# Kernel optimization log

Hardware: AMD Instinct MI355X
Metric: run time of the kernel (lower is better)

Reference implementation:

```python
import jax, jax.numpy as jnp
import numpy as np

NUM_HEADS = 16
NEG_BIG = -1.0e9


def setup_inputs() -> dict:
    key = jax.random.key(0)
    k1, k2, k3 = jax.random.split(key, 3)
    B, S, D = 2, 2048, 1024
    x = jax.random.normal(k1, (B, S, D), dtype=jnp.float32)
    qkv_weights = jax.random.normal(k2, (D, 3 * D), dtype=jnp.float32) * (1.0 / np.sqrt(D))
    output_weights = jax.random.normal(k3, (D, D), dtype=jnp.float32) * (1.0 / np.sqrt(D))
    return {"x": x, "qkv_weights": qkv_weights, "output_weights": output_weights}


def reference(x, qkv_weights, output_weights):
    B, S, D = x.shape
    H = NUM_HEADS
    hd = D // H
    qkv = jnp.einsum('bsd,de->bse', x, qkv_weights)  # [B,S,3D]
    q, k, v = jnp.split(qkv, 3, axis=-1)
    # [B,H,S,hd]
    q = q.reshape(B, S, H, hd).transpose(0, 2, 1, 3)
    k = k.reshape(B, S, H, hd).transpose(0, 2, 1, 3)
    v = v.reshape(B, S, H, hd).transpose(0, 2, 1, 3)
    scores = jnp.einsum('bhqd,bhkd->bhqk', q, k)  # unscaled, matches original masked path
    # original bug: when masked, softmax is applied to UNSCALED scores with mask
    tril = jnp.tril(jnp.ones((S, S), dtype=scores.dtype))
    masked = scores * tril + NEG_BIG * (1.0 - tril)
    attn = jax.nn.softmax(masked, axis=-1)
    heads = jnp.einsum('bhqk,bhkd->bhqd', attn, v)  # [B,H,S,hd]
    merged = heads.transpose(0, 2, 1, 3).reshape(B, S, D)
    return jnp.einsum('bsd,de->bse', merged, output_weights)
```

## Files before the change

### kernel.cpp

```cpp
#include <hip/hip_runtime.h>
#include <stdint.h>

using u16 = unsigned short;
typedef __attribute__((ext_vector_type(8))) _Float16 half8;
typedef __attribute__((ext_vector_type(4))) float f32x4;
typedef __attribute__((ext_vector_type(4))) unsigned short u16x4;

#define S_LEN 2048
#define D_MODEL 1024
#define NHEAD 16
#define HDIM 64

__device__ __forceinline__ u16 f2h_bits(float f){
    _Float16 h = (_Float16)f;
    return __builtin_bit_cast(u16, h);
}

typedef __attribute__((address_space(1))) void gvoid;
typedef __attribute__((address_space(3))) void lvoid;
__device__ __forceinline__ void gload_lds16(const u16* g, u16* l){
    __builtin_amdgcn_global_load_lds((gvoid*)(uintptr_t)g, (lvoid*)l, 16, 0, 0);
}

__global__ __launch_bounds__(256) void k_cvt_x(const float* __restrict__ x, u16* __restrict__ xh){
    int i = blockIdx.x*256 + threadIdx.x;
    float4 v = reinterpret_cast<const float4*>(x)[i];
    u16x4 o;
    o.x = f2h_bits(v.x); o.y = f2h_bits(v.y); o.z = f2h_bits(v.z); o.w = f2h_bits(v.w);
    reinterpret_cast<u16x4*>(xh)[i] = o;
}

__global__ __launch_bounds__(256) void k_cvt_wT(const float* __restrict__ W, u16* __restrict__ WT,
                                                int K, int N){
    __shared__ float t[32][33];
    int tx = threadIdx.x & 31, ty = threadIdx.x >> 5;
    int n0 = blockIdx.x*32, k0 = blockIdx.y*32;
    #pragma unroll
    for (int i=0;i<4;++i) t[ty+8*i][tx] = W[(size_t)(k0+ty+8*i)*N + n0+tx];
    __syncthreads();
    #pragma unroll
    for (int i=0;i<4;++i) WT[(size_t)(n0+ty+8*i)*K + k0+tx] = f2h_bits(t[tx][ty+8*i]);
}

template<int EPI>
__global__ __launch_bounds__(256) void k_gemm(const u16* __restrict__ A, const u16* __restrict__ BT,
                                              float* __restrict__ Cf, u16* __restrict__ Qh,
                                              u16* __restrict__ Kh, u16* __restrict__ Vt){
    constexpr int Kd = 1024;
    __shared__ u16 As[128*32];
    __shared__ u16 Bs[128*32];
    int nwg = gridDim.x;
    int cpx = nwg >> 3;
    int wg  = ((int)blockIdx.x & 7)*cpx + ((int)blockIdx.x >> 3);
    int tm = wg & 31, tn = wg >> 5;
    int t = threadIdx.x;
    int w = t >> 6, lane = t & 63;
    int lr = lane & 15, lg = lane >> 4;
    int wm = (w>>1)*64, wn = (w&1)*64;
    int m0 = tm*128 + wm, n0 = tn*128 + wn;

    const u16* aG = A  + (size_t)(tm*128 + (t>>2))*Kd + (t&3)*8;
    const u16* bG = BT + (size_t)(tn*128 + (t>>2))*Kd + (t&3)*8;
    u16* aL = As + (t>>2)*32 + (t&3)*8;
    u16* bL = Bs + (t>>2)*32 + (t&3)*8;

    f32x4 acc[4][4];
    #pragma unroll
    for (int i=0;i<4;++i)
        #pragma unroll
        for (int j=0;j<4;++j) acc[i][j] = (f32x4){0.f,0.f,0.f,0.f};

    for (int kk=0; kk<Kd; kk+=32){
        gload_lds16(aG + kk, aL);
        gload_lds16(aG + kk + (size_t)64*Kd, aL + 64*32);
        gload_lds16(bG + kk, bL);
        gload_lds16(bG + kk + (size_t)64*Kd, bL + 64*32);
        __syncthreads();

        half8 av[4], bv[4];
        #pragma unroll
        for (int mf=0;mf<4;++mf) av[mf] = *reinterpret_cast<const half8*>(&As[(wm+mf*16+lr)*32 + lg*8]);
        #pragma unroll
        for (int nf=0;nf<4;++nf) bv[nf] = *reinterpret_cast<const half8*>(&Bs[(wn+nf*16+lr)*32 + lg*8]);
        __builtin_amdgcn_s_setprio(1);
        #pragma unroll
        for (int mf=0;mf<4;++mf)
            #pragma unroll
            for (int nf=0;nf<4;++nf)
                acc[mf][nf] = __builtin_amdgcn_mfma_f32_16x16x32_f16(av[mf], bv[nf], acc[mf][nf], 0,0,0);
        __builtin_amdgcn_s_setprio(0);
        __syncthreads();
    }

    if (EPI == 0){
        #pragma unroll
        for (int mf=0;mf<4;++mf)
            #pragma unroll
            for (int nf=0;nf<4;++nf)
                #pragma unroll
                for (int j=0;j<4;++j)
                    Cf[(size_t)(m0+mf*16+lg*4+j)*D_MODEL + n0+nf*16+lr] = acc[mf][nf][j];
    } else {
        #pragma unroll
        for (int mf=0;mf<4;++mf){
            int r0 = m0 + mf*16 + lg*4;
            int b  = r0 >> 11, s = r0 & 2047;
            #pragma unroll
            for (int nf=0;nf<4;++nf){
                int col = n0 + nf*16 + lr;
                int which = col >> 10;
                int d  = col & 1023;
                int h  = d >> 6, di = d & 63;
                int bh = b*NHEAD + h;
                if (which == 2){
                    u16x4 pv;
                    pv.x = f2h_bits(acc[mf][nf][0]);
                    pv.y = f2h_bits(acc[mf][nf][1]);
                    pv.z = f2h_bits(acc[mf][nf][2]);
                    pv.w = f2h_bits(acc[mf][nf][3]);
                    *reinterpret_cast<u16x4*>(Vt + ((size_t)bh*HDIM + di)*S_LEN + s) = pv;
                } else {
                    u16* dst = (which==0 ? Qh : Kh) + ((size_t)bh*S_LEN + s)*HDIM + di;
                    #pragma unroll
                    for (int j=0;j<4;++j) dst[(size_t)j*HDIM] = f2h_bits(acc[mf][nf][j]);
                }
            }
        }
    }
}

__global__ __launch_bounds__(256,3) void k_attn(const u16* __restrict__ Q, const u16* __restrict__ K,
                                                const u16* __restrict__ Vt, u16* __restrict__ Mg){
    __shared__ u16 Kl[64*64];
    __shared__ u16 Vl[64*64];
    __shared__ u16 plds[4][32][72];
    int t = threadIdx.x;
    int w = t >> 6, lane = t & 63;
    int lr = lane & 15, lg = lane >> 4;
    int blk = blockIdx.x;
    int bh  = blk & 31;
    int g   = blk >> 5;
    int qb  = (g < 8) ? g : 23 - g;
    int q0w = qb*128 + w*32;
    int b = bh >> 4, h = bh & 15;
    const u16* Qp = Q  + (size_t)bh*S_LEN*HDIM;
    const u16* Kp = K  + (size_t)bh*S_LEN*HDIM;
    const u16* Vp = Vt + (size_t)bh*HDIM*S_LEN;

    int c0 = t, c1 = t + 256;
    int r0 = c0 >> 3, s0 = 8*((c0 & 7) ^ (r0 & 7));
    int r1 = c1 >> 3, s1 = 8*((c1 & 7) ^ (r1 & 7));
    const u16* Ks0 = Kp + (size_t)r0*HDIM + s0;
    const u16* Ks1 = Kp + (size_t)r1*HDIM + s1;
    const u16* Vs0 = Vp + (size_t)r0*S_LEN + s0;
    const u16* Vs1 = Vp + (size_t)r1*S_LEN + s1;
    u16* Kd0 = Kl + c0*8; u16* Kd1 = Kl + c1*8;
    u16* Vd0 = Vl + c0*8; u16* Vd1 = Vl + c1*8;

    half8 qf[2][2];
    #pragma unroll
    for (int qi=0;qi<2;++qi)
        #pragma unroll
        for (int ks=0;ks<2;++ks){
            half8 v = *reinterpret_cast<const half8*>(Qp + (size_t)(q0w+qi*16+lr)*HDIM + ks*32 + lg*8);
            #pragma unroll
            for (int j=0;j<8;++j) v[j] = v[j] * (_Float16)1.44269504f;
            qf[qi][ks] = v;
        }

    f32x4 oacc[2][4];
    float mrow[2], lrow[2];
    #pragma unroll
    for (int mf=0;mf<2;++mf){
        #pragma unroll
        for (int nf=0;nf<4;++nf) oacc[mf][nf] = (f32x4){0.f,0.f,0.f,0.f};
        mrow[mf] = -1e30f; lrow[mf] = 0.f;
    }

    int ktb    = 2*qb + 2;
    int lastkt = (q0w + 31) >> 6;

    int swz = (lr & 7)*8;

    for (int kt=0; kt<ktb; ++kt){
        int kbase = kt*64;
        gload_lds16(Ks0 + (size_t)kbase*HDIM, Kd0);
        gload_lds16(Ks1 + (size_t)kbase*HDIM, Kd1);
        gload_lds16(Vs0 + kbase, Vd0);
        gload_lds16(Vs1 + kbase, Vd1);
        __syncthreads();

        if (kt <= lastkt){
            half8 kfr[4][2];
            #pragma unroll
            for (int kf=0;kf<4;++kf)
                #pragma unroll
                for (int ks=0;ks<2;++ks)
                    kfr[kf][ks] = *reinterpret_cast<const half8*>(Kl + (kf*16+lr)*64 + ((ks*32 + lg*8) ^ swz));
            f32x4 sc[4][2];
            #pragma unroll
            for (int kf=0;kf<4;++kf)
                #pragma unroll
                for (int qi=0;qi<2;++qi) sc[kf][qi] = (f32x4){0.f,0.f,0.f,0.f};
            __builtin_amdgcn_s_setprio(1);
            #pragma unroll
            for (int kf=0;kf<4;++kf)
                #pragma unroll
                for (int qi=0;qi<2;++qi)
                    #pragma unroll
                    for (int ks=0;ks<2;++ks)
                        sc[kf][qi] = __builtin_amdgcn_mfma_f32_16x16x32_f16(kfr[kf][ks], qf[qi][ks], sc[kf][qi], 0,0,0);
            __builtin_amdgcn_s_setprio(0);

            half8 vf[4][2];
            #pragma unroll
            for (int nf=0;nf<4;++nf)
                #pragma unroll
                for (int kh=0;kh<2;++kh)
                    vf[nf][kh] = *reinterpret_cast<const half8*>(Vl + (nf*16+lr)*64 + ((kh*32 + lg*8) ^ swz));

            if (kt == lastkt){
                #pragma unroll
                for (int kf=0;kf<4;++kf)
                    #pragma unroll
                    for (int qi=0;qi<2;++qi)
                        #pragma unroll
                        for (int j=0;j<4;++j)
                            if (kbase+kf*16+lg*4+j > q0w+qi*16+lr) sc[kf][qi][j] = -1e9f;
            }

            float pmax[2];
            #pragma unroll
            for (int qi=0;qi<2;++qi){
                float t0 = fmaxf(fmaxf(sc[0][qi][0], sc[0][qi][1]), fmaxf(sc[0][qi][2], sc[0][qi][3]));
                float t1 = fmaxf(fmaxf(sc[1][qi][0], sc[1][qi][1]), fmaxf(sc[1][qi][2], sc[1][qi][3]));
                float t2 = fmaxf(fmaxf(sc[2][qi][0], sc[2][qi][1]), fmaxf(sc[2][qi][2], sc[2][qi][3]));
                float t3 = fmaxf(fmaxf(sc[3][qi][0], sc[3][qi][1]), fmaxf(sc[3][qi][2], sc[3][qi][3]));
                float tm = fmaxf(fmaxf(t0,t1), fmaxf(t2,t3));
                tm = fmaxf(tm, __shfl_xor(tm,16));
                tm = fmaxf(tm, __shfl_xor(tm,32));
                pmax[qi] = tm;
            }
            bool need = (pmax[0] > mrow[0]+8.0f) || (pmax[1] > mrow[1]+8.0f);
            if (__any(need)){
                float aq[2];
                #pragma unroll
                for (int qi=0;qi<2;++qi){
                    float mnew = fmaxf(mrow[qi], pmax[qi]);
                    aq[qi] = __builtin_amdgcn_exp2f(mrow[qi] - mnew);
                    mrow[qi] = mnew;
                    lrow[qi] *= aq[qi];
                }
                float am[2][4];
                #pragma unroll
                for (int mf=0;mf<2;++mf)
                    #pragma unroll
                    for (int j=0;j<4;++j) am[mf][j] = __shfl(aq[mf], lg*4+j);
                #pragma unroll
                for (int mf=0;mf<2;++mf)
                    #pragma unroll
                    for (int nf=0;nf<4;++nf)
                        #pragma unroll
                        for (int j=0;j<4;++j) oacc[mf][nf][j] *= am[mf][j];
            }
            #pragma unroll
            for (int qi=0;qi<2;++qi){
                float m = mrow[qi];
                float rs = 0.f;
                #pragma unroll
                for (int kf=0;kf<4;++kf)
                    #pragma unroll
                    for (int j=0;j<4;++j){
                        float e = __builtin_amdgcn_exp2f(sc[kf][qi][j] - m);
                        sc[kf][qi][j] = e;
                        rs += e;
                    }
                rs += __shfl_xor(rs,16);
                rs += __shfl_xor(rs,32);
                lrow[qi] += rs;
            }
            #pragma unroll
            for (int kf=0;kf<4;++kf)
                #pragma unroll
                for (int qi=0;qi<2;++qi){
                    u16x4 pk;
                    pk.x = f2h_bits(sc[kf][qi][0]);
                    pk.y = f2h_bits(sc[kf][qi][1]);
                    pk.z = f2h_bits(sc[kf][qi][2]);
                    pk.w = f2h_bits(sc[kf][qi][3]);
                    *reinterpret_cast<u16x4*>(&plds[w][qi*16+lr][kf*16+lg*4]) = pk;
                }
            half8 pa[2][2];
            #pragma unroll
            for (int mf=0;mf<2;++mf)
                #pragma unroll
                for (int kh=0;kh<2;++kh)
                    pa[mf][kh] = *reinterpret_cast<const half8*>(&plds[w][mf*16+lr][kh*32 + lg*8]);
            __builtin_amdgcn_s_setprio(1);
            #pragma unroll
            for (int mf=0;mf<2;++mf)
                #pragma unroll
                for (int nf=0;nf<4;++nf)
                    #pragma unroll
                    for (int kh=0;kh<2;++kh)
                        oacc[mf][nf] = __builtin_amdgcn_mfma_f32_16x16x32_f16(pa[mf][kh], vf[nf][kh], oacc[mf][nf], 0,0,0);
            __builtin_amdgcn_s_setprio(0);
        }
        __syncthreads();
    }

    float linv[2][4];
    #pragma unroll
    for (int mf=0;mf<2;++mf)
        #pragma unroll
        for (int j=0;j<4;++j) linv[mf][j] = 1.0f/__shfl(lrow[mf], lg*4+j);
    #pragma unroll
    for (int mf=0;mf<2;++mf)
        #pragma unroll
        for (int nf=0;nf<4;++nf)
            #pragma unroll
            for (int j=0;j<4;++j)
                Mg[(size_t)(b*S_LEN + q0w + mf*16 + lg*4 + j)*D_MODEL + h*HDIM + nf*16 + lr]
                    = f2h_bits(oacc[mf][nf][j]*linv[mf][j]);
}

extern "C" void kernel_launch(void* const* d_in, const int* in_sizes, int n_in,
                              void* d_out, int out_size, void* d_ws, size_t ws_size,
                              hipStream_t stream) {
    const float* x    = (const float*)d_in[0];
    const float* wqkv = (const float*)d_in[1];
    const float* wout = (const float*)d_in[2];
    float* out = (float*)d_out;
    char* ws = (char*)d_ws;

    const size_t MB = 1u<<20;
    u16* xh     = (u16*)(ws + 0*MB);
    u16* wqkvT  = (u16*)(ws + 8*MB);
    u16* woutT  = (u16*)(ws + 14*MB);
    u16* Qh     = (u16*)(ws + 16*MB);
    u16* Kh     = (u16*)(ws + 24*MB);
    u16* Vt     = (u16*)(ws + 32*MB);
    u16* Mg     = (u16*)(ws + 40*MB);

    k_cvt_x <<<4096, 256, 0, stream>>>(x, xh);
    k_cvt_wT<<<dim3(96,32), 256, 0, stream>>>(wqkv, wqkvT, 1024, 3072);
    k_cvt_wT<<<dim3(32,32), 256, 0, stream>>>(wout, woutT, 1024, 1024);
    k_gemm<1><<<768, 256, 0, stream>>>(xh, wqkvT, nullptr, Qh, Kh, Vt);
    k_attn  <<<512, 256, 0, stream>>>(Qh, Kh, Vt, Mg);
    k_gemm<0><<<256, 256, 0, stream>>>(Mg, woutT, out, nullptr, nullptr, nullptr);
}
```

Measured before the change: 134.1 us.

## Split long causal attention rows across two blocks and merge partials

Query blocks 8-15, which have the longest causal key ranges, are now each split into two workgroups covering halves of the key range. Each half writes a normalized fp16 partial output plus its row max and sum, and a new combine kernel merges them with log-sum-exp weights. This aims to balance work across 768 workgroups instead of 512 so the longest blocks no longer set the tail. The cost is an extra kernel launch, extra global traffic for the partials, and fp16 rounding of the intermediate outputs.

```diff
diff --git a/kernel.cpp b/kernel.cpp
--- a/kernel.cpp
+++ b/kernel.cpp
@@ -14,6 +14,9 @@
 __device__ __forceinline__ u16 f2h_bits(float f){
     _Float16 h = (_Float16)f;
     return __builtin_bit_cast(u16, h);
+}
+__device__ __forceinline__ float h2f_bits(u16 v){
+    return (float)__builtin_bit_cast(_Float16, v);
 }
 
 typedef __attribute__((address_space(1))) void gvoid;
@@ -130,7 +133,9 @@
 }
 
 __global__ __launch_bounds__(256,3) void k_attn(const u16* __restrict__ Q, const u16* __restrict__ K,
-                                                const u16* __restrict__ Vt, u16* __restrict__ Mg){
+                                                const u16* __restrict__ Vt, u16* __restrict__ Mg,
+                                                u16* __restrict__ On, float* __restrict__ Ml,
+                                                float* __restrict__ Ll){
     __shared__ u16 Kl[64*64];
     __shared__ u16 Vl[64*64];
     __shared__ u16 plds[4][32][72];
@@ -139,10 +144,14 @@
     int lr = lane & 15, lg = lane >> 4;
     int blk = blockIdx.x;
     int bh  = blk & 31;
-    int g   = blk >> 5;
-    int qb  = (g < 8) ? g : 23 - g;
+    int p   = blk >> 5;
+    int qb, ktLo, ktHi, part; bool split;
+    if (p < 8)      { qb = p;    ktLo = 0;      ktHi = 2*p+2;   split = false; part = 0; }
+    else if (p < 16){ qb = 23-p; ktLo = 0;      ktHi = qb+1;    split = true;  part = 0; }
+    else            { qb = 31-p; ktLo = qb+1;   ktHi = 2*qb+2;  split = true;  part = 1; }
     int q0w = qb*128 + w*32;
     int b = bh >> 4, h = bh & 15;
+    int pid = split ? ((bh<<3) + (qb-8))*2 + part : 0;
     const u16* Qp = Q  + (size_t)bh*S_LEN*HDIM;
     const u16* Kp = K  + (size_t)bh*S_LEN*HDIM;
     const u16* Vp = Vt + (size_t)bh*HDIM*S_LEN;
@@ -177,12 +186,10 @@
         mrow[mf] = -1e30f; lrow[mf] = 0.f;
     }
 
-    int ktb    = 2*qb + 2;
     int lastkt = (q0w + 31) >> 6;
-
     int swz = (lr & 7)*8;
 
-    for (int kt=0; kt<ktb; ++kt){
+    for (int kt=ktLo; kt<ktHi; ++kt){
         int kbase = kt*64;
         gload_lds16(Ks0 + (size_t)kbase*HDIM, Kd0);
         gload_lds16(Ks1 + (size_t)kbase*HDIM, Kd1);
@@ -314,14 +321,57 @@
     for (int mf=0;mf<2;++mf)
         #pragma unroll
         for (int j=0;j<4;++j) linv[mf][j] = 1.0f/__shfl(lrow[mf], lg*4+j);
-    #pragma unroll
-    for (int mf=0;mf<2;++mf)
-        #pragma unroll
-        for (int nf=0;nf<4;++nf)
-            #pragma unroll
-            for (int j=0;j<4;++j)
-                Mg[(size_t)(b*S_LEN + q0w + mf*16 + lg*4 + j)*D_MODEL + h*HDIM + nf*16 + lr]
-                    = f2h_bits(oacc[mf][nf][j]*linv[mf][j]);
+    if (!split){
+        #pragma unroll
+        for (int mf=0;mf<2;++mf)
+            #pragma unroll
+            for (int nf=0;nf<4;++nf)
+                #pragma unroll
+                for (int j=0;j<4;++j)
+                    Mg[(size_t)(b*S_LEN + q0w + mf*16 + lg*4 + j)*D_MODEL + h*HDIM + nf*16 + lr]
+                        = f2h_bits(oacc[mf][nf][j]*linv[mf][j]);
+    } else {
+        #pragma unroll
+        for (int mf=0;mf<2;++mf)
+            #pragma unroll
+            for (int nf=0;nf<4;++nf)
+                #pragma unroll
+                for (int j=0;j<4;++j)
+                    On[pid*8192 + (w*32 + mf*16 + lg*4 + j)*64 + nf*16 + lr]
+                        = f2h_bits(oacc[mf][nf][j]*linv[mf][j]);
+        if (lg == 0){
+            #pragma unroll
+            for (int qi=0;qi<2;++qi){
+                Ml[pid*128 + w*32 + qi*16 + lr] = mrow[qi];
+                Ll[pid*128 + w*32 + qi*16 + lr] = lrow[qi];
+            }
+        }
+    }
+}
+
+__global__ __launch_bounds__(256) void k_comb(const u16* __restrict__ On, const float* __restrict__ Ml,
+                                              const float* __restrict__ Ll, u16* __restrict__ Mg){
+    int blk = blockIdx.x;
+    int bh = blk & 31;
+    int q8 = blk >> 5;
+    int qb = 8 + q8;
+    int b = bh >> 4, h = bh & 15;
+    int t = threadIdx.x;
+    int c = t & 63, rg = t >> 6;
+    int pid0 = ((bh<<3) + q8)*2, pid1 = pid0 + 1;
+    #pragma unroll 4
+    for (int i=0;i<32;++i){
+        int r = rg*32 + i;
+        float m1 = Ml[pid0*128 + r], m2 = Ml[pid1*128 + r];
+        float l1 = Ll[pid0*128 + r], l2 = Ll[pid1*128 + r];
+        float M  = fmaxf(m1, m2);
+        float w1 = l1*__builtin_amdgcn_exp2f(m1 - M);
+        float w2 = l2*__builtin_amdgcn_exp2f(m2 - M);
+        float o1 = h2f_bits(On[pid0*8192 + r*64 + c]);
+        float o2 = h2f_bits(On[pid1*8192 + r*64 + c]);
+        float o  = (w1*o1 + w2*o2) / (w1 + w2);
+        Mg[(size_t)(b*S_LEN + qb*128 + r)*D_MODEL + h*HDIM + c] = f2h_bits(o);
+    }
 }
 
 extern "C" void kernel_launch(void* const* d_in, const int* in_sizes, int n_in,
@@ -341,11 +391,15 @@
     u16* Kh     = (u16*)(ws + 24*MB);
     u16* Vt     = (u16*)(ws + 32*MB);
     u16* Mg     = (u16*)(ws + 40*MB);
+    u16* On     = (u16*)(ws + 48*MB);
+    float* Ml   = (float*)(ws + 56*MB);
+    float* Ll   = (float*)(ws + 56*MB + 256*1024);
 
     k_cvt_x <<<4096, 256, 0, stream>>>(x, xh);
     k_cvt_wT<<<dim3(96,32), 256, 0, stream>>>(wqkv, wqkvT, 1024, 3072);
     k_cvt_wT<<<dim3(32,32), 256, 0, stream>>>(wout, woutT, 1024, 1024);
     k_gemm<1><<<768, 256, 0, stream>>>(xh, wqkvT, nullptr, Qh, Kh, Vt);
-    k_attn  <<<512, 256, 0, stream>>>(Qh, Kh, Vt, Mg);
+    k_attn  <<<768, 256, 0, stream>>>(Qh, Kh, Vt, Mg, On, Ml, Ll);
+    k_comb  <<<256, 256, 0, stream>>>(On, Ml, Ll, Mg);
     k_gemm<0><<<256, 256, 0, stream>>>(Mg, woutT, out, nullptr, nullptr, nullptr);
 }
```

New measurement: 129.5 us. 1.04x faster.
